# Kernel tuning notes

Hardware: AMD Instinct MI355X
Metric: run time of the kernel (lower is better)

The kernel has to match this reference:

```python
import jax, jax.numpy as jnp
import numpy as np
import math

H, D, S, B = 8, 512, 2048, 2
DH = D // H  # hidden_dim = 64
REL_CLIP = 2048


def setup_inputs() -> dict:
    key = jax.random.key(0)
    ks = jax.random.split(key, 6)
    def xavier(k, shape):
        fan_in, fan_out = shape[-2], shape[-1]
        a = math.sqrt(6.0 / (fan_in + fan_out))
        return jax.random.uniform(k, shape, jnp.float32, -a, a)
    return {
        "X": jax.random.normal(ks[0], (B, S, D), jnp.float32),
        "mask": jnp.zeros((S, S), jnp.float32),
        "Wq": xavier(ks[1], (H, D, DH)),
        "Wk": xavier(ks[2], (H, D, DH)),
        "Wv": xavier(ks[3], (H, D, DH)),
        "Wo": xavier(ks[4], (D, D)),
        "att_rel_emb": xavier(ks[5], (H, DH, REL_CLIP)),
    }


def _skew(rel):
    # rel: [H, B, S, S] -> Transformer-XL skewing trick
    h, b, s, _ = rel.shape
    relflat = rel.reshape(h * b, s, s)
    padded = jnp.pad(relflat, ((0, 0), (0, 0), (1, 0)))       # [H*B, S, S+1]
    reshaped = padded.reshape(h * b, s + 1, s)                 # [H*B, S+1, S]
    return reshaped[:, 1:, :].reshape(h, b, s, s)


def reference(X, mask, Wq, Wk, Wv, Wo, att_rel_emb):
    batch, seq, model_dim = X.shape
    num_heads, _, hidden_dim = Wq.shape
    scale = 1.0 / math.sqrt(hidden_dim)
    q = jnp.einsum("bsm,hmd->hbsd", X, Wq) * scale
    k = jnp.einsum("bsm,hmd->hbsd", X, Wk)
    v = jnp.einsum("bsm,hmd->hbsd", X, Wv)
    logits = jnp.einsum("hbsd,hbtd->hbst", q, k)               # [H,B,S,S]
    ErT = att_rel_emb[:, :, att_rel_emb.shape[-1] - seq:]      # [H,DH,S]
    rel = jnp.einsum("hbsd,hdt->hbst", q, ErT)
    Srel = _skew(rel)
    logits = logits + Srel + mask
    attn = jax.nn.softmax(logits, axis=-1)
    out = jnp.einsum("hbst,hbtd->hbsd", attn, v)               # [H,B,S,DH]
    out = out.transpose(1, 2, 0, 3).reshape(batch, seq, num_heads * hidden_dim)
    return out @ Wo
```

## Files before the change

kernel.cpp:

```cpp
#include <hip/hip_runtime.h>
#include <hip/hip_bf16.h>

typedef unsigned short u16;
typedef unsigned int   u32;
typedef __attribute__((ext_vector_type(8))) short bf16x8;
typedef __attribute__((ext_vector_type(4))) float f32x4;

#define DEVI static __device__ __forceinline__

DEVI u16 f2bf(float f){
  u32 u = __float_as_uint(f);
  u = (u + 0x7fffu + ((u >> 16) & 1u)) >> 16;
  return (u16)u;
}
DEVI float bf2f(u16 h){ return __uint_as_float(((u32)h) << 16); }

DEVI u32 pk2(float a, float b){
  u32 r;
  asm("v_cvt_pk_bf16_f32 %0, %1, %2" : "=v"(r) : "v"(a), "v"(b));
  return r;
}
DEVI u16 cvt1(float f){ return (u16)pk2(f, f); }

DEVI int swz(int row, int col){ return row*64 + (col ^ ((row & 7) << 3)); }

DEVI void stage64(u16* __restrict__ lds, const u16* __restrict__ g, int ld){
  int tid = threadIdx.x;
  #pragma unroll
  for (int c = tid; c < 512; c += 256){
    int row = c >> 3;
    int col = (c & 7) << 3;
    int4 v = *(const int4*)(g + (size_t)row*ld + col);
    *(int4*)(lds + swz(row, col)) = v;
  }
}

DEVI void gload16(const u16* g, u16* l){
  typedef __attribute__((address_space(1))) u16 gu16;
  typedef __attribute__((address_space(3))) u16 lu16;
  __builtin_amdgcn_global_load_lds((gu16*)g, (lu16*)l, 16, 0, 0);
}

DEVI void stage64a(u16* lds, const u16* g, int ld){
  int w = threadIdx.x >> 6, l = threadIdx.x & 63;
  #pragma unroll
  for (int i = 0; i < 2; ++i){
    int e = (w*2 + i)*512 + l*8;
    int row = e >> 6, col = e & 63;
    gload16(g + (size_t)row*ld + (col ^ ((row & 7) << 3)), lds + (w*2 + i)*512);
  }
}

DEVI void stageEWa(u16* lds, const u16* Eg, int diff0){
  int w = threadIdx.x >> 6, l = threadIdx.x & 63;
  #pragma unroll
  for (int i = 0; i < 4; ++i){
    int e = (w*4 + i)*512 + l*8;
    int row = e >> 6, col = e & 63;
    bool useA = (diff0 < 0) | ((diff0 == 0) & (row < 64));
    int j = row + diff0 + (useA ? 1984 : -65);
    j = j < 0 ? 0 : (j > 2047 ? 2047 : j);
    gload16(Eg + (size_t)j*64 + (col ^ ((row & 7) << 3)), lds + (w*4 + i)*512);
  }
}

DEVI bf16x8 ldsfrag(const u16* lds, int row, int k){
  union { int4 i; bf16x8 b; } u;
  u.i = *(const int4*)(lds + swz(row, k));
  return u.b;
}

DEVI float rmax16(float v){
  #pragma unroll
  for (int m = 1; m < 16; m <<= 1) v = fmaxf(v, __shfl_xor(v, m, 16));
  return v;
}
DEVI float rsum16(float v){
  #pragma unroll
  for (int m = 1; m < 16; m <<= 1) v += __shfl_xor(v, m, 16);
  return v;
}

__global__ void k_castX(const float4* __restrict__ X, ushort4* __restrict__ Xb, int n4){
  int i = blockIdx.x*256 + threadIdx.x;
  if (i >= n4) return;
  float4 v = X[i];
  ushort4 o; o.x = f2bf(v.x); o.y = f2bf(v.y); o.z = f2bf(v.z); o.w = f2bf(v.w);
  Xb[i] = o;
}

__global__ void k_packW(const float* __restrict__ Wq, const float* __restrict__ Wk,
                        const float* __restrict__ Wv, u16* __restrict__ Wt){
  int i = blockIdx.x*256 + threadIdx.x;
  if (i >= 1536*512) return;
  int n = i >> 9, m = i & 511;
  int sel = n >> 9, hd = n & 511;
  int h = hd >> 6, d = hd & 63;
  const float* W = (sel == 0) ? Wq : ((sel == 1) ? Wk : Wv);
  Wt[i] = f2bf(W[((size_t)h*512 + m)*64 + d]);
}

__global__ void k_packWo(const float* __restrict__ Wo, u16* __restrict__ Wot){
  int i = blockIdx.x*256 + threadIdx.x;
  if (i >= 512*512) return;
  int n = i >> 9, m = i & 511;
  Wot[i] = f2bf(Wo[(size_t)m*512 + n]);
}

__global__ void k_packEr(const float* __restrict__ Er, u16* __restrict__ ErT){
  int i = blockIdx.x*256 + threadIdx.x;
  if (i >= 8*2048*64) return;
  int h = i >> 17, r = i & 131071;
  int t = r >> 6, d = r & 63;
  ErT[i] = f2bf(Er[((size_t)h*64 + d)*2048 + t]);
}

DEVI void gemm_core(const u16* __restrict__ Ag, int lda,
                    const u16* __restrict__ Bg, int ldb, int K,
                    u16* Alds, u16* Blds, f32x4 acc[4])
{
  int w = threadIdx.x >> 6, l = threadIdx.x & 63;
  int arow = w*16 + (l & 15);
  int kof  = (l >> 4) * 8;
  for (int k0 = 0; k0 < K; k0 += 64){
    __syncthreads();
    stage64(Alds, Ag + k0, lda);
    stage64(Blds, Bg + k0, ldb);
    __syncthreads();
    #pragma unroll
    for (int ks = 0; ks < 2; ++ks){
      bf16x8 a = ldsfrag(Alds, arow, ks*32 + kof);
      #pragma unroll
      for (int ct = 0; ct < 4; ++ct){
        bf16x8 b = ldsfrag(Blds, ct*16 + (l & 15), ks*32 + kof);
        acc[ct] = __builtin_amdgcn_mfma_f32_16x16x32_bf16(a, b, acc[ct], 0, 0, 0);
      }
    }
  }
}

__global__ __launch_bounds__(256) void k_gemm_qkv(
  const u16* __restrict__ X, const u16* __restrict__ Wt,
  u16* __restrict__ Q, u16* __restrict__ Ko, u16* __restrict__ Vn)
{
  __shared__ u16 Alds[64*64], Blds[64*64];
  int m0 = blockIdx.y * 64, n0 = blockIdx.x * 64;
  f32x4 acc[4];
  #pragma unroll
  for (int i = 0; i < 4; ++i) acc[i] = (f32x4){0.f,0.f,0.f,0.f};
  gemm_core(X + (size_t)m0*512, 512, Wt + (size_t)n0*512, 512, 512, Alds, Blds, acc);

  int w = threadIdx.x >> 6, l = threadIdx.x & 63;
  int rbase = m0 + w*16 + ((l >> 4) << 2);
  #pragma unroll
  for (int ct = 0; ct < 4; ++ct){
    int col = n0 + ct*16 + (l & 15);
    int sel = col >> 9;
    int hd  = col & 511;
    int h = hd >> 6, d = hd & 63;
    #pragma unroll
    for (int r = 0; r < 4; ++r){
      int row = rbase + r;
      int b = row >> 11, s = row & 2047;
      float v = acc[ct][r];
      if (sel == 0)      Q [(((size_t)(h*2 + b))*2048 + s)*64 + d] = f2bf(v * 0.125f);
      else if (sel == 1) Ko[(((size_t)(h*2 + b))*2048 + s)*64 + d] = f2bf(v);
      else               Vn[((size_t)row)*512 + hd] = f2bf(v);
    }
  }
}

__global__ __launch_bounds__(256) void k_transV(const u16* __restrict__ Vn, u16* __restrict__ Vt){
  __shared__ u16 t[64][72];
  int hb = blockIdx.y, h = hb >> 1, b = hb & 1;
  int s0 = blockIdx.x * 64;
  int tid = threadIdx.x;
  for (int c = tid; c < 512; c += 256){
    int sr = c >> 3, col = (c & 7) << 3;
    int4 v = *(const int4*)(Vn + ((size_t)(b*2048 + s0 + sr))*512 + h*64 + col);
    *(int4*)(&t[sr][col]) = v;
  }
  __syncthreads();
  for (int c = tid; c < 512; c += 256){
    int dr = c >> 3, col = (c & 7) << 3;
    union { u16 e[8]; int4 v; } tmp;
    #pragma unroll
    for (int j = 0; j < 8; ++j) tmp.e[j] = t[col + j][dr];
    *(int4*)(Vt + ((size_t)(hb*64 + dr))*2048 + s0 + col) = tmp.v;
  }
}

__global__ __launch_bounds__(256) void k_attn(
  const u16* __restrict__ Q, const u16* __restrict__ Kg_, const u16* __restrict__ Vt,
  const u16* __restrict__ ErT, const float* __restrict__ mask, u16* __restrict__ AO)
{
  __shared__ u16 QsPs[66*64];
  __shared__ u16 Ks[2*64*64];
  __shared__ u16 Vs[2*64*64];
  __shared__ u16 EW[128*64];
  __shared__ u16 Rs[4*80*16];

  int tid = threadIdx.x;
  int w = tid >> 6, l = tid & 63;
  int hb = blockIdx.y, h = hb >> 1, b = hb & 1;
  int p0 = blockIdx.x * 64;
  const u16* Qg  = Q   + (size_t)hb*2048*64;
  const u16* Kgg = Kg_ + (size_t)hb*2048*64;
  const u16* Vg  = Vt  + (size_t)hb*64*2048;
  const u16* Eg  = ErT + (size_t)h*2048*64;

  stage64a(Ks, Kgg, 64);
  stage64a(Vs, Vg, 2048);
  stageEWa(EW, Eg, -p0);

  for (int c = tid; c < 520; c += 256){
    int row = c >> 3, col = (c & 7) << 3;
    int gr = p0 + row; if (gr > 2047) gr = 2047;
    *(int4*)(QsPs + swz(row, col)) = *(const int4*)(Qg + (size_t)gr*64 + col);
  }
  __syncthreads();

  int kof = (l >> 4) * 8;
  int l15 = l & 15;
  int arow = w*16 + l15;
  int ribase = (l >> 4) * 4;
  bf16x8 qa0 = ldsfrag(QsPs, arow,     kof);
  bf16x8 qa1 = ldsfrag(QsPs, arow,     32 + kof);
  bf16x8 qb0 = ldsfrag(QsPs, arow + 1, kof);
  bf16x8 qb1 = ldsfrag(QsPs, arow + 1, 32 + kof);

  float mrun[4], lrun[4];
  f32x4 o[4];
  #pragma unroll
  for (int r = 0; r < 4; ++r){ mrun[r] = -1e30f; lrun[r] = 0.f; }
  #pragma unroll
  for (int dt = 0; dt < 4; ++dt) o[dt] = (f32x4){0.f,0.f,0.f,0.f};

  u16* Rw = Rs + w*1280;
  int p = 0;

  for (int t0 = 0; t0 < 2048; t0 += 64){
    int diff0 = t0 - p0;
    const u16* Ksp = Ks + p*4096;
    const u16* Vsp = Vs + p*4096;

    float mk[4][4];
    #pragma unroll
    for (int ct = 0; ct < 4; ++ct){
      #pragma unroll
      for (int r = 0; r < 4; ++r)
        mk[ct][r] = mask[(size_t)(p0 + w*16 + ribase + r)*2048 + t0 + ct*16 + l15];
    }

    if (t0 < 1984){
      stage64a(Ks + (p^1)*4096, Kgg + (size_t)(t0 + 64)*64, 64);
      stage64a(Vs + (p^1)*4096, Vg + (t0 + 64), 2048);
    }

    float sv[4][4];
    #pragma unroll
    for (int ct = 0; ct < 4; ++ct){
      f32x4 s = (f32x4){0.f,0.f,0.f,0.f};
      s = __builtin_amdgcn_mfma_f32_16x16x32_bf16(qa0, ldsfrag(Ksp, ct*16 + l15, kof),      s, 0, 0, 0);
      s = __builtin_amdgcn_mfma_f32_16x16x32_bf16(qa1, ldsfrag(Ksp, ct*16 + l15, 32 + kof), s, 0, 0, 0);
      #pragma unroll
      for (int r = 0; r < 4; ++r) sv[ct][r] = s[r];
    }

    {
      bool allB = diff0 > 0, diag = diff0 == 0;
      #pragma unroll
      for (int j5 = 0; j5 < 5; ++j5){
        int ct2 = (3 - w) + j5;
        bool useB = allB | (diag & (ct2 >= 4));
        f32x4 rr = (f32x4){0.f,0.f,0.f,0.f};
        rr = __builtin_amdgcn_mfma_f32_16x16x32_bf16(useB ? qb0 : qa0, ldsfrag(EW, ct2*16 + l15, kof),      rr, 0, 0, 0);
        rr = __builtin_amdgcn_mfma_f32_16x16x32_bf16(useB ? qb1 : qa1, ldsfrag(EW, ct2*16 + l15, 32 + kof), rr, 0, 0, 0);
        uint2 pv;
        pv.x = pk2(rr[0], rr[1]);
        pv.y = pk2(rr[2], rr[3]);
        *(uint2*)(Rw + (j5*16 + l15)*16 + ribase) = pv;
      }
    }

    __builtin_amdgcn_s_barrier();
    if (t0 < 1984) stageEWa(EW, Eg, diff0 + 64);

    #pragma unroll
    for (int ct = 0; ct < 4; ++ct){
      int ti = ct*16 + l15;
      #pragma unroll
      for (int r = 0; r < 4; ++r){
        int pl = ribase + r;
        int rg = diff0 + ti - (w*16 + pl);
        float srl = bf2f(Rw[(15 + ti - pl)*16 + pl]);
        srl = (rg == 1) ? 0.f : srl;
        sv[ct][r] += mk[ct][r] + srl;
      }
    }

    #pragma unroll
    for (int r = 0; r < 4; ++r){
      float tm = fmaxf(fmaxf(sv[0][r], sv[1][r]), fmaxf(sv[2][r], sv[3][r]));
      tm = rmax16(tm);
      float mn = fmaxf(mrun[r], tm);
      float corr = __expf(mrun[r] - mn);
      mrun[r] = mn;
      lrun[r] *= corr;
      #pragma unroll
      for (int dt = 0; dt < 4; ++dt) o[dt][r] *= corr;
      float ps = 0.f;
      #pragma unroll
      for (int ct = 0; ct < 4; ++ct){
        float pv = __expf(sv[ct][r] - mn);
        ps += pv;
        QsPs[swz(w*16 + ribase + r, ct*16 + l15)] = cvt1(pv);
      }
      lrun[r] += rsum16(ps);
    }

    #pragma unroll
    for (int ks = 0; ks < 2; ++ks){
      bf16x8 pa = ldsfrag(QsPs, arow, ks*32 + kof);
      #pragma unroll
      for (int dt = 0; dt < 4; ++dt){
        bf16x8 vb = ldsfrag(Vsp, dt*16 + l15, ks*32 + kof);
        o[dt] = __builtin_amdgcn_mfma_f32_16x16x32_bf16(pa, vb, o[dt], 0, 0, 0);
      }
    }

    __syncthreads();
    p ^= 1;
  }

  #pragma unroll
  for (int r = 0; r < 4; ++r){
    float inv = 1.0f / lrun[r];
    int pp = p0 + w*16 + ribase + r;
    #pragma unroll
    for (int dt = 0; dt < 4; ++dt)
      AO[((size_t)(b*2048 + pp))*512 + h*64 + dt*16 + l15] = cvt1(o[dt][r] * inv);
  }
}

__global__ __launch_bounds__(256) void k_gemm_wo(
  const u16* __restrict__ AO, const u16* __restrict__ Wot, float* __restrict__ out)
{
  __shared__ u16 Alds[64*64], Blds[64*64];
  int m0 = blockIdx.y * 64, n0 = blockIdx.x * 64;
  f32x4 acc[4];
  #pragma unroll
  for (int i = 0; i < 4; ++i) acc[i] = (f32x4){0.f,0.f,0.f,0.f};
  gemm_core(AO + (size_t)m0*512, 512, Wot + (size_t)n0*512, 512, 512, Alds, Blds, acc);

  int w = threadIdx.x >> 6, l = threadIdx.x & 63;
  int rbase = m0 + w*16 + ((l >> 4) << 2);
  #pragma unroll
  for (int ct = 0; ct < 4; ++ct){
    int col = n0 + ct*16 + (l & 15);
    #pragma unroll
    for (int r = 0; r < 4; ++r)
      out[(size_t)(rbase + r)*512 + col] = acc[ct][r];
  }
}

extern "C" void kernel_launch(void* const* d_in, const int* in_sizes, int n_in,
                              void* d_out, int out_size, void* d_ws, size_t ws_size,
                              hipStream_t stream)
{
  const float* X    = (const float*)d_in[0];
  const float* mask = (const float*)d_in[1];
  const float* Wq   = (const float*)d_in[2];
  const float* Wk   = (const float*)d_in[3];
  const float* Wv   = (const float*)d_in[4];
  const float* Wo   = (const float*)d_in[5];
  const float* Er   = (const float*)d_in[6];
  float* out = (float*)d_out;

  char* p = (char*)d_ws;
  auto carve = [&](size_t bytes)->char*{ char* r = p; p += (bytes + 255) & ~(size_t)255; return r; };
  u16* Xbf = (u16*)carve(4096ull*512*2);
  u16* Wt  = (u16*)carve(1536ull*512*2);
  u16* Wot = (u16*)carve(512ull*512*2);
  u16* ErT = (u16*)carve(8ull*2048*64*2);
  u16* Qb  = (u16*)carve(16ull*2048*64*2);
  u16* Kb  = (u16*)carve(16ull*2048*64*2);
  u16* Vn  = (u16*)carve(4096ull*512*2);
  u16* Vt  = (u16*)carve(16ull*64*2048*2);
  u16* AO  = (u16*)carve(4096ull*512*2);

  k_castX  <<<dim3(2048), dim3(256), 0, stream>>>((const float4*)X, (ushort4*)Xbf, 524288);
  k_packW  <<<dim3(3072), dim3(256), 0, stream>>>(Wq, Wk, Wv, Wt);
  k_packWo <<<dim3(1024), dim3(256), 0, stream>>>(Wo, Wot);
  k_packEr <<<dim3(4096), dim3(256), 0, stream>>>(Er, ErT);

  k_gemm_qkv<<<dim3(24, 64), dim3(256), 0, stream>>>(Xbf, Wt, Qb, Kb, Vn);
  k_transV  <<<dim3(32, 16), dim3(256), 0, stream>>>(Vn, Vt);
  k_attn    <<<dim3(32, 16), dim3(256), 0, stream>>>(Qb, Kb, Vt, ErT, mask, AO);
  k_gemm_wo <<<dim3(8, 64), dim3(256), 0, stream>>>(AO, Wot, out);

  (void)in_sizes; (void)n_in; (void)out_size; (void)ws_size;
}
```

Before: 168.0 us.

## Write unnormalized attention partials and normalize in a separate combine kernel

The attention kernel now stores unnormalized fp32 outputs plus per-row max and sum into reused workspace buffers, and a new combine kernel normalizes them and writes bf16 AO. Grid and per-block work are unchanged, so it adds no split-KV parallelism. It only adds an extra kernel launch and extra fp32 global traffic. It looks like scaffolding for a later split along the key dimension.

```diff
diff --git a/kernel.cpp b/kernel.cpp
--- a/kernel.cpp
+++ b/kernel.cpp
@@ -192,7 +192,8 @@
 
 __global__ __launch_bounds__(256) void k_attn(
   const u16* __restrict__ Q, const u16* __restrict__ Kg_, const u16* __restrict__ Vt,
-  const u16* __restrict__ ErT, const float* __restrict__ mask, u16* __restrict__ AO)
+  const u16* __restrict__ ErT, const float* __restrict__ mask,
+  float* __restrict__ Op0, float* __restrict__ Op1, float2* __restrict__ ML)
 {
   __shared__ u16 QsPs[66*64];
   __shared__ u16 Ks[2*64*64];
@@ -202,7 +203,7 @@
 
   int tid = threadIdx.x;
   int w = tid >> 6, l = tid & 63;
-  int hb = blockIdx.y, h = hb >> 1, b = hb & 1;
+  int hb = blockIdx.y, h = hb >> 1;
   int p0 = blockIdx.x * 64;
   const u16* Qg  = Q   + (size_t)hb*2048*64;
   const u16* Kgg = Kg_ + (size_t)hb*2048*64;
@@ -333,14 +334,37 @@
     p ^= 1;
   }
 
+  float* Up = (hb < 8) ? (Op0 + (size_t)hb*2048*64)
+                       : (Op1 + (size_t)(hb - 8)*2048*64);
   #pragma unroll
   for (int r = 0; r < 4; ++r){
-    float inv = 1.0f / lrun[r];
     int pp = p0 + w*16 + ribase + r;
     #pragma unroll
     for (int dt = 0; dt < 4; ++dt)
-      AO[((size_t)(b*2048 + pp))*512 + h*64 + dt*16 + l15] = cvt1(o[dt][r] * inv);
-  }
+      Up[(size_t)pp*64 + dt*16 + l15] = o[dt][r];
+    if (l15 == 0) ML[(size_t)hb*2048 + pp] = make_float2(mrun[r], lrun[r]);
+  }
+}
+
+__global__ __launch_bounds__(256) void k_comb(
+  const float* __restrict__ Op0, const float* __restrict__ Op1,
+  const float2* __restrict__ ML, u16* __restrict__ AO)
+{
+  int i = blockIdx.x*256 + threadIdx.x;
+  int d8 = i & 7, row = (i >> 3) & 2047, hb = i >> 14;
+  int h = hb >> 1, b = hb & 1;
+  const float* Up = (hb < 8) ? (Op0 + (size_t)hb*2048*64)
+                             : (Op1 + (size_t)(hb - 8)*2048*64);
+  float2 a = ML[(size_t)hb*2048 + row];
+  float inv = 1.f / a.y;
+  const float4* x = (const float4*)(Up + (size_t)row*64 + d8*8);
+  float4 x0 = x[0], x1 = x[1];
+  union { u16 e[8]; int4 v; } outv;
+  outv.e[0] = cvt1(x0.x * inv); outv.e[1] = cvt1(x0.y * inv);
+  outv.e[2] = cvt1(x0.z * inv); outv.e[3] = cvt1(x0.w * inv);
+  outv.e[4] = cvt1(x1.x * inv); outv.e[5] = cvt1(x1.y * inv);
+  outv.e[6] = cvt1(x1.z * inv); outv.e[7] = cvt1(x1.w * inv);
+  *(int4*)(AO + ((size_t)(b*2048 + row))*512 + h*64 + d8*8) = outv.v;
 }
 
 __global__ __launch_bounds__(256) void k_gemm_wo(
@@ -389,6 +413,10 @@
   u16* Vt  = (u16*)carve(16ull*64*2048*2);
   u16* AO  = (u16*)carve(4096ull*512*2);
 
+  float*  Op0 = (float*)Xbf;
+  float*  Op1 = (float*)Vn;
+  float2* MLb = (float2*)Wt;
+
   k_castX  <<<dim3(2048), dim3(256), 0, stream>>>((const float4*)X, (ushort4*)Xbf, 524288);
   k_packW  <<<dim3(3072), dim3(256), 0, stream>>>(Wq, Wk, Wv, Wt);
   k_packWo <<<dim3(1024), dim3(256), 0, stream>>>(Wo, Wot);
@@ -396,7 +424,8 @@
 
   k_gemm_qkv<<<dim3(24, 64), dim3(256), 0, stream>>>(Xbf, Wt, Qb, Kb, Vn);
   k_transV  <<<dim3(32, 16), dim3(256), 0, stream>>>(Vn, Vt);
-  k_attn    <<<dim3(32, 16), dim3(256), 0, stream>>>(Qb, Kb, Vt, ErT, mask, AO);
+  k_attn    <<<dim3(32, 16), dim3(256), 0, stream>>>(Qb, Kb, Vt, ErT, mask, Op0, Op1, MLb);
+  k_comb    <<<dim3(1024), dim3(256), 0, stream>>>(Op0, Op1, MLb, AO);
   k_gemm_wo <<<dim3(8, 64), dim3(256), 0, stream>>>(AO, Wot, out);
 
   (void)in_sizes; (void)n_in; (void)out_size; (void)ws_size;
```

New measurement: 173.6 us. 3.4% more time.
